# Optimization experiments

Hardware: AMD Instinct MI355X
Metric: run time of the kernel (lower is better)

The kernel has to match this reference:

```python
import jax, jax.numpy as jnp
import numpy as np

B, N, MODES, WIDTH = 4, 8192, 12, 32
TWO = 2 * MODES  # 24
M_TOT = TWO * (TWO - 1)  # 552


def setup_inputs() -> dict:
    key = jax.random.key(0)
    ks = jax.random.split(key, 12)
    scale = 1.0 / (WIDTH * WIDTH)
    x = jax.random.uniform(ks[0], (B, N, 2), jnp.float32)
    fc0_w = jax.random.normal(ks[1], (2, WIDTH), jnp.float32) * 0.1
    fc0_b = jax.random.normal(ks[2], (WIDTH,), jnp.float32) * 0.05
    # 4 layers x {weights1, weights2}, stored as real/imag pairs (torch.rand cfloat ~ U[0,1)+1j*U[0,1))
    spec_w = jax.random.uniform(ks[3], (4, 2, WIDTH, WIDTH, MODES, MODES, 2), jnp.float32) * scale
    conv_w = jax.random.normal(ks[4], (4, WIDTH, WIDTH), jnp.float32) * 0.1  # Conv1d k=1 -> [O,I]
    conv_b = jax.random.normal(ks[5], (4, WIDTH), jnp.float32) * 0.05
    fc1_w = jax.random.normal(ks[6], (WIDTH, 128), jnp.float32) * 0.1
    fc1_b = jax.random.normal(ks[7], (128,), jnp.float32) * 0.05
    fc2_w = jax.random.normal(ks[8], (128, 1), jnp.float32) * 0.1
    fc2_b = jax.random.normal(ks[9], (1,), jnp.float32) * 0.05
    return {"x": x, "fc0_w": fc0_w, "fc0_b": fc0_b, "spec_w": spec_w,
            "conv_w": conv_w, "conv_b": conv_b, "fc1_w": fc1_w, "fc1_b": fc1_b,
            "fc2_w": fc2_w, "fc2_b": fc2_b}


def _vft_matrices(xp, yp):
    # xp, yp: [B, N], already min-shifted and scaled to [0, 6.28]
    kx = jnp.concatenate([jnp.arange(MODES), jnp.arange(-MODES, 0)]).astype(jnp.float32)       # [24]
    ky = jnp.concatenate([jnp.arange(MODES), jnp.arange(-(MODES - 1), 0)]).astype(jnp.float32)  # [23]
    Xm = kx[None, :, None] * xp[:, None, :]  # [B,24,N]
    Ym = ky[None, :, None] * yp[:, None, :]  # [B,23,N]
    # torch: X repeat(1,23,1) tiles blocks; Y repeat(1,1,24).reshape interleaves -> row j*24+i = X[i]+Y[j]
    phase = jnp.tile(Xm, (1, TWO - 1, 1)) + jnp.repeat(Ym, TWO, axis=1)  # [B,552,N]
    V_fwd = jnp.exp(-1j * phase)                    # [B,552,N] complex64
    V_inv = jnp.conj(V_fwd).transpose(0, 2, 1)      # [B,N,552]
    return V_fwd, V_inv


def _spectral_conv(h, V_fwd, V_inv, w1, w2):
    # h: [B,C,N] real; w1,w2: [C,C,M,M] complex
    b, c, n = h.shape
    # forward Vandermonde transform: bmm(V_fwd, h^T) then permute -> [B,C,552]
    x_ft = jnp.einsum('bmn,bnc->bcm', V_fwd, h.astype(jnp.complex64).transpose(0, 2, 1))
    x_ft = x_ft.reshape(b, c, TWO, TWO - 1)
    top = jnp.einsum('bixy,ioxy->boxy', x_ft[:, :, :MODES, :MODES], w1)
    bot = jnp.einsum('bixy,ioxy->boxy', x_ft[:, :, -MODES:, :MODES], w2)
    out_ft = jnp.zeros((b, WIDTH, TWO, MODES), jnp.complex64)
    out_ft = out_ft.at[:, :, :MODES, :MODES].set(top)
    out_ft = out_ft.at[:, :, -MODES:, :MODES].set(bot)
    x_ft = out_ft.reshape(b, WIDTH, 2 * MODES * MODES)  # [B,C,288]
    # conjugate-symmetric completion (flip over last two dims, as in source)
    x_ft2 = jnp.conj(jnp.flip(x_ft[..., TWO:], axis=(-2, -1)))  # [B,C,264]
    x_ft = jnp.concatenate([x_ft, x_ft2], axis=-1)  # [B,C,552]
    out = jnp.einsum('bnm,bmc->bcn', V_inv, x_ft.transpose(0, 2, 1))  # [B,C,N]
    return (out / n * 2).real


def reference(x, fc0_w, fc0_b, spec_w, conv_w, conv_b, fc1_w, fc1_b, fc2_w, fc2_b):
    gelu = lambda t: jax.nn.gelu(t, approximate=False)
    # VFT mutates x in-place by subtracting global mins (view semantics in torch)
    xp = x[:, :, 0] - jnp.min(x[:, :, 0])
    yp = x[:, :, 1] - jnp.min(x[:, :, 1])
    x_in = jnp.stack([xp, yp], axis=-1)  # what fc0 actually sees
    V_fwd, V_inv = _vft_matrices(xp * 6.28 / jnp.max(xp), yp * 6.28 / jnp.max(yp))
    h = (x_in @ fc0_w + fc0_b).transpose(0, 2, 1)  # [B,C,N]
    for l in range(4):
        w1 = spec_w[l, 0, ..., 0] + 1j * spec_w[l, 0, ..., 1]
        w2 = spec_w[l, 1, ..., 0] + 1j * spec_w[l, 1, ..., 1]
        x1 = _spectral_conv(h, V_fwd, V_inv, w1, w2)
        x2 = jnp.einsum('bin,oi->bon', h, conv_w[l]) + conv_b[l][None, :, None]
        h = x1 + x2
        if l < 3:
            h = gelu(h)
    h = h.transpose(0, 2, 1)  # [B,N,C]
    h = gelu(h @ fc1_w + fc1_b)
    return h @ fc2_w + fc2_b  # [B,N,1]
```

## Files before the change

kernel.cpp:

```cpp
#include <hip/hip_runtime.h>
#include <cmath>

#define NB 4
#define NN 8192
#define CH 32

typedef short short8 __attribute__((ext_vector_type(8)));
typedef float floatx4 __attribute__((ext_vector_type(4)));
typedef unsigned short ushort_t;

__device__ __forceinline__ unsigned short f2b(float f){
  unsigned u = __float_as_uint(f);
  u = u + 0x7FFFu + ((u >> 16) & 1u);
  return (unsigned short)(u >> 16);
}
__device__ __forceinline__ float b2f(unsigned short h){
  return __uint_as_float(((unsigned)h) << 16);
}
__device__ __forceinline__ float gelu_f(float v){
  return 0.5f * v * (1.0f + erff(v * 0.70710678118654752440f));
}
__device__ __forceinline__ int repk(int t){
  int j = t / 24, i = t - j * 24;
  if(j == 0)  return (i <= 12) ? i : -1;
  if(j <= 11) return 13 + (j - 1) * 24 + i;
  return (i == 12) ? 277 + (j - 12) : -1;
}
__device__ __forceinline__ int partner(int t){
  int j = t / 24, i = t - j * 24;
  return ((23 - j) % 23) * 24 + ((24 - i) % 24);
}
__device__ __forceinline__ int repT(int k){
  if(k < 13) return k;
  if(k < 277){ int m = k - 13; return (m / 24 + 1) * 24 + (m % 24); }
  return (k - 277 + 12) * 24 + 12;
}

__global__ __launch_bounds__(256) void k_pre(const float* __restrict__ spec,
    float2* __restrict__ wt, const float* __restrict__ x, float4* __restrict__ pmm,
    const float* __restrict__ fc1w, ushort_t* __restrict__ WB,
    const float* __restrict__ convw, ushort_t* __restrict__ WA)
{
  const int tid = threadIdx.x;
  if(blockIdx.x < 128){
    int g = blockIdx.x * 256 + tid;
    float a = x[(size_t)g * 2], b = x[(size_t)g * 2 + 1];
    float mn0 = a, mx0 = a, mn1 = b, mx1 = b;
    for(int off = 32; off > 0; off >>= 1){
      mn0 = fminf(mn0, __shfl_down(mn0, off));
      mx0 = fmaxf(mx0, __shfl_down(mx0, off));
      mn1 = fminf(mn1, __shfl_down(mn1, off));
      mx1 = fmaxf(mx1, __shfl_down(mx1, off));
    }
    __shared__ float4 wp[4];
    if((tid & 63) == 0) wp[tid >> 6] = make_float4(mn0, mn1, mx0, mx1);
    __syncthreads();
    if(tid == 0){
      float4 r = wp[0];
      for(int i2 = 1; i2 < 4; ++i2){
        float4 v = wp[i2];
        r.x = fminf(r.x, v.x); r.y = fminf(r.y, v.y);
        r.z = fmaxf(r.z, v.z); r.w = fmaxf(r.w, v.w);
      }
      pmm[blockIdx.x] = r;
    }
  } else if(blockIdx.x < 4736){
    int g = (blockIdx.x - 128) * 256 + tid;
    int o  = g & 31;
    int i  = (g >> 5) & 31;
    int rest = g >> 10;
    int pq = rest % 144;
    int ls = rest / 144;
    wt[g] = ((const float2*)spec)[(((size_t)(ls * 32 + i) * 32 + o) * 144 + pq)];
  } else {
    for(int s = tid; s < 512; s += 256){
      int jt = s >> 6, l = s & 63;
      int c = l & 15, qq = l >> 4;
      #pragma unroll
      for(int e = 0; e < 8; ++e){
        float wv = fc1w[(qq * 8 + e) * 128 + jt * 16 + c];
        ushort_t hi = f2b(wv);
        WB[(jt * 64 + l) * 8 + e] = hi;
        WB[4096 + (jt * 64 + l) * 8 + e] = f2b(wv - b2f(hi));
      }
    }
    for(int s = tid; s < 8192; s += 256){
      int l2   = s >> 11;
      int rem  = s & 2047;
      int limb = rem >> 10;
      int rem2 = rem & 1023;
      int half = rem2 >> 9;
      int le   = rem2 & 511;
      int lane = le >> 3, e = le & 7;
      int c = half * 16 + (lane & 15);
      int i = (lane >> 4) * 8 + e;
      float wv = convw[((size_t)l2 * 32 + c) * 32 + i] * 4096.0f;
      ushort_t hi = f2b(wv);
      WA[s] = limb ? f2b(wv - b2f(hi)) : hi;
    }
  }
}

__global__ __launch_bounds__(256) void k_vbuild(const float* __restrict__ x,
    const float4* __restrict__ pmm, const float* __restrict__ fw,
    const float* __restrict__ fb, ushort_t* __restrict__ AF, ushort_t* __restrict__ VTF,
    ushort_t* __restrict__ hbB, ushort_t* __restrict__ hbChi, ushort_t* __restrict__ hbClo)
{
  __shared__ ushort_t lds1[32 * 584];
  __shared__ float4 mmv;
  const int tid = threadIdx.x;
  if(tid < 64){
    float4 a = pmm[tid], c = pmm[tid + 64];
    float mn0 = fminf(a.x, c.x), mn1 = fminf(a.y, c.y);
    float mx0 = fmaxf(a.z, c.z), mx1 = fmaxf(a.w, c.w);
    for(int off = 32; off > 0; off >>= 1){
      mn0 = fminf(mn0, __shfl_down(mn0, off));
      mn1 = fminf(mn1, __shfl_down(mn1, off));
      mx0 = fmaxf(mx0, __shfl_down(mx0, off));
      mx1 = fmaxf(mx1, __shfl_down(mx1, off));
    }
    if(tid == 0) mmv = make_float4(mn0, mn1, mx0, mx1);
  }
  __syncthreads();
  const int nl = tid & 31, part = tid >> 5;
  const int b = blockIdx.x >> 8;
  const int nblk = blockIdx.x & 255;
  const int n = nblk * 32 + nl;
  float mn0 = mmv.x, mn1 = mmv.y, mx0 = mmv.z, mx1 = mmv.w;
  float x0 = x[(size_t)(b * NN + n) * 2]     - mn0;
  float x1 = x[(size_t)(b * NN + n) * 2 + 1] - mn1;
  float sp = x0 * (6.28f / (mx0 - mn0));
  float sq = x1 * (6.28f / (mx1 - mn1));
  float cx, sx, cy, sy;
  sincosf(sp, &sx, &cx);
  sincosf(sq, &sy, &cy);
  int j0 = part * 3;
  int j1 = (j0 + 3 < 23) ? j0 + 3 : 23;
  float ky0 = (j0 < 12) ? (float)j0 : (float)(j0 - 23);
  float cb, sb;
  sincosf(ky0 * sq, &sb, &cb);
  for(int j = j0; j < j1; ++j){
    float ca = 1.0f, sa = 0.0f;
    #pragma unroll
    for(int i = 0; i < 24; ++i){
      float vr = ca * cb - sa * sb;
      float vi = -(sa * cb + ca * sb);
      int t = j * 24 + i;
      int k = repk(t);
      if(k >= 0){
        lds1[nl * 584 + k]       = f2b(vr);
        lds1[nl * 584 + 288 + k] = f2b(vi);
      }
      float cn = ca * cx - sa * sx;
      float sn = sa * cx + ca * sx;
      if(i == 11) sn = -sn;
      ca = cn; sa = sn;
    }
    float cbn = cb * cy - sb * sy;
    float sbn = sb * cy + cb * sy;
    cb = cbn; sb = sbn;
  }
  __syncthreads();
  #pragma unroll
  for(int r = 0; r < 9; ++r){
    int c = tid + 256 * r;
    int t16 = c / 1152;
    int c2 = c - t16 * 1152;
    int kk = c2 >> 6;
    int rem = c2 & 63;
    int q = rem >> 4, n15 = rem & 15;
    short8 v = *(const short8*)(lds1 + (t16 * 16 + n15) * 584 + kk * 32 + q * 8);
    *(short8*)(VTF + ((size_t)((b * 512 + nblk * 2 + t16) * 18 + kk)) * 512
               + (q * 16 + n15) * 8) = v;
  }
  #pragma unroll
  for(int r = 0; r < 9; ++r){
    int c = tid + 256 * r;
    int st = c >> 6;
    int rem = c & 63;
    int q = rem >> 4, srow = rem & 15;
    int sg = st * 16 + srow;
    int s = (sg < 288) ? sg : sg - 288;
    int sinh_ = (sg >= 288);
    int p2 = s / 12, qq = s - p2 * 12;
    int t = p2 * 23 + qq;
    int k = repk(t);
    unsigned short flip = 0;
    if(k < 0){ k = repk(partner(t)); if(sinh_) flip = 0x8000; }
    int col = sinh_ ? 288 + k : k;
    ushort_t tmp[8];
    #pragma unroll
    for(int e = 0; e < 8; ++e)
      tmp[e] = lds1[(q * 8 + e) * 584 + col] ^ flip;
    *(short8*)(AF + ((size_t)((b * 36 + st) * 256 + nblk)) * 512
               + (q * 16 + srow) * 8) = *(short8*)tmp;
  }
  #pragma unroll
  for(int rr = 0; rr < 4; ++rr){
    int c2 = part + rr * 8;
    float v = fb[c2] + x0 * fw[c2] + x1 * fw[32 + c2];
    ushort_t hi = f2b(v), lo = f2b(v - b2f(hi));
    int half = c2 >> 4, cl = c2 & 15;
    hbB[(((size_t)(b * 2 + half) * 256 + nblk) * 512) + ((nl >> 3) * 16 + cl) * 8 + (nl & 7)] = hi;
    size_t ca = ((size_t)(b * 512 + nblk * 2 + (nl >> 4))) * 512
              + ((c2 >> 3) * 16 + (nl & 15)) * 8 + (c2 & 7);
    hbChi[ca] = hi; hbClo[ca] = lo;
  }
}

__global__ __launch_bounds__(256) void k_fwd(const ushort_t* __restrict__ AF,
    const ushort_t* __restrict__ hbB, float* __restrict__ xp)
{
  const int stp = blockIdx.x;
  const int ks = blockIdx.y;
  const int b  = blockIdx.z;
  const int w = threadIdx.x >> 6;
  const int lane = threadIdx.x & 63;
  const int row = lane & 15;
  const int q = lane >> 4;
  const int st0 = stp * 2;
  const size_t abase0 = ((size_t)(b * 36 + st0) * 256) * 512 + (q * 16 + row) * 8;
  const size_t abase1 = abase0 + (size_t)256 * 512;
  const size_t hB0 = ((size_t)(b * 2 + 0) * 256) * 512 + (size_t)lane * 8;
  const size_t hB1 = ((size_t)(b * 2 + 1) * 256) * 512 + (size_t)lane * 8;
  floatx4 aA0 = {0.f,0.f,0.f,0.f}, aA1 = {0.f,0.f,0.f,0.f};
  floatx4 aB0 = {0.f,0.f,0.f,0.f}, aB1 = {0.f,0.f,0.f,0.f};
  #pragma unroll
  for(int kk = 0; kk < 4; ++kk){
    int g = ks * 16 + w * 4 + kk;
    short8 A0 = *(const short8*)(AF + abase0 + (size_t)g * 512);
    short8 A1 = *(const short8*)(AF + abase1 + (size_t)g * 512);
    short8 B0 = *(const short8*)(hbB + hB0 + (size_t)g * 512);
    short8 B1 = *(const short8*)(hbB + hB1 + (size_t)g * 512);
    aA0 = __builtin_amdgcn_mfma_f32_16x16x32_bf16(A0, B0, aA0, 0, 0, 0);
    aA1 = __builtin_amdgcn_mfma_f32_16x16x32_bf16(A0, B1, aA1, 0, 0, 0);
    aB0 = __builtin_amdgcn_mfma_f32_16x16x32_bf16(A1, B0, aB0, 0, 0, 0);
    aB1 = __builtin_amdgcn_mfma_f32_16x16x32_bf16(A1, B1, aB1, 0, 0, 0);
  }
  __shared__ float red[4 * 512];
  const int e = threadIdx.x;
  const int eo = e & 31;
  #pragma unroll
  for(int r = 0; r < 4; ++r){
    int rrow = q * 4 + r;
    red[w * 512 + rrow * 32 + row]      = aA0[r];
    red[w * 512 + rrow * 32 + 16 + row] = aA1[r];
  }
  __syncthreads();
  {
    float v0 = red[e] + red[512 + e] + red[1024 + e] + red[1536 + e];
    float v1 = red[e + 256] + red[512 + e + 256] + red[1024 + e + 256] + red[1536 + e + 256];
    size_t r0 = (size_t)(b * 576 + st0 * 16 + (e >> 5));
    xp[(r0 * 16 + ks) * 32 + eo]       = v0;
    xp[((r0 + 8) * 16 + ks) * 32 + eo] = v1;
  }
  __syncthreads();
  #pragma unroll
  for(int r = 0; r < 4; ++r){
    int rrow = q * 4 + r;
    red[w * 512 + rrow * 32 + row]      = aB0[r];
    red[w * 512 + rrow * 32 + 16 + row] = aB1[r];
  }
  __syncthreads();
  {
    float v0 = red[e] + red[512 + e] + red[1024 + e] + red[1536 + e];
    float v1 = red[e + 256] + red[512 + e + 256] + red[1024 + e + 256] + red[1536 + e + 256];
    size_t r0 = (size_t)(b * 576 + (st0 + 1) * 16 + (e >> 5));
    xp[(r0 * 16 + ks) * 32 + eo]       = v0;
    xp[((r0 + 8) * 16 + ks) * 32 + eo] = v1;
  }
}

__global__ __launch_bounds__(256) void k_mixg(const float* __restrict__ xp,
    const float2* __restrict__ wt, ushort_t* __restrict__ ghi, ushort_t* __restrict__ glof,
    int layer)
{
  const int w = threadIdx.x >> 6;
  const int lane = threadIdx.x & 63;
  const int k = blockIdx.x * 4 + w;
  const int b = blockIdx.y;
  const int t = repT(k);
  const int j = t / 24, i = t - j * 24;
  const int u = partner(t);
  const bool unpaired = (i == 12) || (u == t);
  const int idxT = (t < 288) ? t : 575 - t;  const bool cfT = (t >= 288);
  const int idxU = (u < 288) ? u : 575 - u;  const bool cfU = (u >= 288);
  __shared__ float Xs[4][2][64];
  #pragma unroll
  for(int m = 0; m < 2; ++m){
    int idx = m ? idxU : idxT;
    #pragma unroll
    for(int hf = 0; hf < 2; ++hf){
      int rrow = hf ? 288 + idx : idx;
      const float* sb = xp + (size_t)(b * 576 + rrow) * 512;
      float4 a = *(const float4*)(sb + lane * 4);
      float4 c = *(const float4*)(sb + 256 + lane * 4);
      a.x += c.x; a.y += c.y; a.z += c.z; a.w += c.w;
      #pragma unroll
      for(int mk = 8; mk <= 32; mk <<= 1){
        a.x += __shfl_xor(a.x, mk);
        a.y += __shfl_xor(a.y, mk);
        a.z += __shfl_xor(a.z, mk);
        a.w += __shfl_xor(a.w, mk);
      }
      if(lane < 8){
        int o0 = hf * 32 + lane * 4;
        Xs[w][m][o0 + 0] = a.x;
        Xs[w][m][o0 + 1] = a.y;
        Xs[w][m][o0 + 2] = a.z;
        Xs[w][m][o0 + 3] = a.w;
      }
    }
  }
  __syncthreads();
  const int o = lane & 31, half = lane >> 5;
  float Fr[2], Fi[2];
  #pragma unroll
  for(int m = 0; m < 2; ++m){
    int idx = m ? idxU : idxT;
    int p2 = idx / 12, qq = idx - p2 * 12;
    int sel = (p2 < 12) ? 0 : 1;
    int pq = (p2 % 12) * 12 + qq;
    const float2* wb = wt + ((size_t)((layer * 2 + sel) * 144 + pq)) * 1024;
    int i0 = half * 16;
    float fr = 0.f, fi = 0.f;
    #pragma unroll
    for(int ii = 0; ii < 16; ++ii){
      int i2 = i0 + ii;
      float xr = Xs[w][m][i2], xi = Xs[w][m][32 + i2];
      float2 wv = wb[i2 * 32 + o];
      fr += xr * wv.x - xi * wv.y;
      fi += xr * wv.y + xi * wv.x;
    }
    fr += __shfl_down(fr, 32);
    fi += __shfl_down(fi, 32);
    Fr[m] = fr; Fi[m] = fi;
  }
  const int c = lane & 31;
  const int srcT = cfT ? 31 - c : c;
  const int srcU = cfU ? 31 - c : c;
  float fax = __shfl(Fr[0], srcT);
  float fay = __shfl(Fi[0], srcT);
  float fbx = __shfl(Fr[1], srcU);
  float fby = __shfl(Fi[1], srcU);
  if(lane < 32){
    float gr = fax;
    float gi = cfT ? -fay : fay;
    if(!unpaired){
      gr += fbx;
      gi -= (cfU ? -fby : fby);
    }
    unsigned short hr = f2b(gr); float lr = gr - b2f(hr);
    unsigned short hi2 = f2b(gi); float li = gi - b2f(hi2);
    size_t base = (size_t)(b * CH + c) * 576;
    ghi[base + k] = hr;          ghi[base + 288 + k] = hi2;
    int hhc = c >> 4, cl = c & 15;
    int kk1 = k >> 5, q1 = (k >> 3) & 3, e1 = k & 7;
    size_t fb2 = (size_t)(b * 2 + hhc) * 18;
    glof[(fb2 + kk1) * 512 + (q1 * 16 + cl) * 8 + e1]     = f2b(lr);
    glof[(fb2 + 9 + kk1) * 512 + (q1 * 16 + cl) * 8 + e1] = f2b(li);
  }
}

template<int LAST>
__global__ __launch_bounds__(512, 6) void k_inv(const ushort_t* __restrict__ VTF,
    const ushort_t* __restrict__ ghi, const ushort_t* __restrict__ glof,
    const float* __restrict__ cbias, int layer,
    const ushort_t* __restrict__ hbCi_hi, const ushort_t* __restrict__ hbCi_lo,
    ushort_t* __restrict__ hbBo, ushort_t* __restrict__ hbCo_hi,
    ushort_t* __restrict__ hbCo_lo,
    const float* __restrict__ b1, const float* __restrict__ w2,
    const float* __restrict__ b2, float* __restrict__ out,
    const ushort_t* __restrict__ WBg, const ushort_t* __restrict__ WA)
{
  __shared__ ushort_t GH[32][584];
  const int tid = threadIdx.x;
  const int b = blockIdx.y;
  const int bx = blockIdx.x;
  for(int idx = tid; idx < 2304; idx += 512){
    int ch = idx / 72, g8 = (idx - ch * 72) * 8;
    if(g8 < 576)
      *(short8*)&GH[ch][g8] = *(const short8*)(ghi + (size_t)(b * CH + ch) * 576 + g8);
  }
  __syncthreads();
  const int lane = tid & 63;
  const int w = tid >> 6;
  const int tl = w >> 1;
  const int hh = w & 1;
  const int row = lane & 15, q = lane >> 4;
  const int t16 = bx * 4 + tl;
  const ushort_t* vb = VTF + ((size_t)(b * 512 + t16) * 18) * 512 + lane * 8;
  const ushort_t* gl = glof + ((size_t)(b * 2 + hh) * 18) * 512 + lane * 8;
  const int gr = hh * 16 + row, ko = q * 8;
  floatx4 ah = {0.f,0.f,0.f,0.f}, al = {0.f,0.f,0.f,0.f};
  #pragma unroll
  for(int kk = 0; kk < 18; ++kk){
    short8 Bv = *(const short8*)(vb + (size_t)kk * 512);
    short8 Ah = *(const short8*)&GH[gr][ko + kk * 32];
    short8 Al = *(const short8*)(gl + (size_t)kk * 512);
    ah = __builtin_amdgcn_mfma_f32_16x16x32_bf16(Ah, Bv, ah, 0, 0, 0);
    al = __builtin_amdgcn_mfma_f32_16x16x32_bf16(Al, Bv, al, 0, 0, 0);
  }
  {
    short8 Whi = *(const short8*)(WA + ((size_t)((layer * 2 + 0) * 2 + hh)) * 512 + lane * 8);
    short8 Wlo = *(const short8*)(WA + ((size_t)((layer * 2 + 1) * 2 + hh)) * 512 + lane * 8);
    short8 Bhi = *(const short8*)(hbCi_hi + ((size_t)(b * 512 + t16)) * 512 + lane * 8);
    short8 Blo = *(const short8*)(hbCi_lo + ((size_t)(b * 512 + t16)) * 512 + lane * 8);
    ah = __builtin_amdgcn_mfma_f32_16x16x32_bf16(Whi, Bhi, ah, 0, 0, 0);
    al = __builtin_amdgcn_mfma_f32_16x16x32_bf16(Wlo, Bhi, al, 0, 0, 0);
    ah = __builtin_amdgcn_mfma_f32_16x16x32_bf16(Whi, Blo, ah, 0, 0, 0);
  }
  floatx4 accF = ah + al;
  const float sc = 2.0f / 8192.0f;
  float cb[4];
  #pragma unroll
  for(int r = 0; r < 4; ++r) cb[r] = cbias[layer * 32 + hh * 16 + q * 4 + r];
  if constexpr(!LAST){
    const int n = bx * 64 + tl * 16 + row;
    const int g = n >> 5, qb = (n >> 3) & 3, e2 = n & 7;
    #pragma unroll
    for(int r = 0; r < 4; ++r){
      int c = hh * 16 + q * 4 + r;
      float v = gelu_f(accF[r] * sc + cb[r]);
      ushort_t hi = f2b(v), lo = f2b(v - b2f(hi));
      hbBo[(((size_t)(b * 2 + hh) * 256 + g) * 512) + (qb * 16 + (q * 4 + r)) * 8 + e2] = hi;
      size_t ca = ((size_t)(b * 512 + t16)) * 512 + ((c >> 3) * 16 + row) * 8 + (c & 7);
      hbCo_hi[ca] = hi; hbCo_lo[ca] = lo;
    }
  } else {
    __shared__ ushort_t hHi[64][36];
    __shared__ ushort_t hLo[64][36];
    __shared__ float part[2][64];
    {
      ushort_t H[4], L[4];
      #pragma unroll
      for(int r = 0; r < 4; ++r){
        float v = accF[r] * sc + cb[r];
        H[r] = f2b(v); L[r] = f2b(v - b2f(H[r]));
      }
      uint2 uu;
      uu.x = (unsigned)H[0] | ((unsigned)H[1] << 16);
      uu.y = (unsigned)H[2] | ((unsigned)H[3] << 16);
      *(uint2*)&hHi[tl * 16 + row][hh * 16 + q * 4] = uu;
      uu.x = (unsigned)L[0] | ((unsigned)L[1] << 16);
      uu.y = (unsigned)L[2] | ((unsigned)L[3] << 16);
      *(uint2*)&hLo[tl * 16 + row][hh * 16 + q * 4] = uu;
    }
    __syncthreads();
    const int cl = row;
    short8 Ahi = *(const short8*)&hHi[tl * 16 + cl][q * 8];
    short8 Alo = *(const short8*)&hLo[tl * 16 + cl][q * 8];
    float S0 = 0.f, S1 = 0.f, S2 = 0.f, S3 = 0.f;
    #pragma unroll
    for(int jt2 = 0; jt2 < 4; ++jt2){
      int jt = hh * 4 + jt2;
      short8 Bhi = *(const short8*)(WBg + (jt * 64 + lane) * 8);
      short8 Blo = *(const short8*)(WBg + 4096 + (jt * 64 + lane) * 8);
      floatx4 acc = {0.f, 0.f, 0.f, 0.f};
      acc = __builtin_amdgcn_mfma_f32_16x16x32_bf16(Ahi, Bhi, acc, 0, 0, 0);
      acc = __builtin_amdgcn_mfma_f32_16x16x32_bf16(Alo, Bhi, acc, 0, 0, 0);
      acc = __builtin_amdgcn_mfma_f32_16x16x32_bf16(Ahi, Blo, acc, 0, 0, 0);
      float bv = b1[jt * 16 + cl], wv = w2[jt * 16 + cl];
      S0 = fmaf(gelu_f(acc[0] + bv), wv, S0);
      S1 = fmaf(gelu_f(acc[1] + bv), wv, S1);
      S2 = fmaf(gelu_f(acc[2] + bv), wv, S2);
      S3 = fmaf(gelu_f(acc[3] + bv), wv, S3);
    }
    #pragma unroll
    for(int off = 8; off; off >>= 1){
      S0 += __shfl_xor(S0, off, 16);
      S1 += __shfl_xor(S1, off, 16);
      S2 += __shfl_xor(S2, off, 16);
      S3 += __shfl_xor(S3, off, 16);
    }
    if(cl == 0){
      int pb = tl * 16 + q * 4;
      part[hh][pb + 0] = S0;
      part[hh][pb + 1] = S1;
      part[hh][pb + 2] = S2;
      part[hh][pb + 3] = S3;
    }
    __syncthreads();
    if(tid < 64)
      out[(size_t)b * NN + bx * 64 + tid] = part[0][tid] + part[1][tid] + b2[0];
  }
}

extern "C" void kernel_launch(void* const* d_in, const int* in_sizes, int n_in,
                              void* d_out, int out_size, void* d_ws, size_t ws_size,
                              hipStream_t stream)
{
  const float* x      = (const float*)d_in[0];
  const float* fc0_w  = (const float*)d_in[1];
  const float* fc0_b  = (const float*)d_in[2];
  const float* spec_w = (const float*)d_in[3];
  const float* conv_w = (const float*)d_in[4];
  const float* conv_b = (const float*)d_in[5];
  const float* fc1_w  = (const float*)d_in[6];
  const float* fc1_b  = (const float*)d_in[7];
  const float* fc2_w  = (const float*)d_in[8];
  const float* fc2_b  = (const float*)d_in[9];
  float* out = (float*)d_out;

  char* w = (char*)d_ws;
  const size_t OFF_PMM  = 0;
  const size_t OFF_WT   = 4096;
  const size_t OFF_AF   = OFF_WT  + 9437184;
  const size_t OFF_VTF  = OFF_AF  + 37748736;
  const size_t OFF_HB0  = OFF_VTF + 37748736;
  const size_t OFF_HB1  = OFF_HB0 + 2097152;
  const size_t OFF_HC0  = OFF_HB1 + 2097152;
  const size_t OFF_HC1  = OFF_HC0 + 2097152;
  const size_t OFF_HL0  = OFF_HC1 + 2097152;
  const size_t OFF_HL1  = OFF_HL0 + 2097152;
  const size_t OFF_XP   = OFF_HL1 + 2097152;
  const size_t OFF_GHI  = OFF_XP  + 4718592;
  const size_t OFF_GLO  = OFF_GHI + 147456;
  const size_t OFF_WB   = OFF_GLO + 147456;
  const size_t OFF_WA   = OFF_WB  + 16384;

  float4* pmm    = (float4*)(w + OFF_PMM);
  float2* wt     = (float2*)(w + OFF_WT);
  ushort_t* AF   = (ushort_t*)(w + OFF_AF);
  ushort_t* VTF  = (ushort_t*)(w + OFF_VTF);
  ushort_t* hbB[2]  = { (ushort_t*)(w + OFF_HB0), (ushort_t*)(w + OFF_HB1) };
  ushort_t* hbChi[2] = { (ushort_t*)(w + OFF_HC0), (ushort_t*)(w + OFF_HC1) };
  ushort_t* hbClo[2] = { (ushort_t*)(w + OFF_HL0), (ushort_t*)(w + OFF_HL1) };
  float* xp      = (float*)(w + OFF_XP);
  ushort_t* ghi  = (ushort_t*)(w + OFF_GHI);
  ushort_t* glof = (ushort_t*)(w + OFF_GLO);
  ushort_t* WB   = (ushort_t*)(w + OFF_WB);
  ushort_t* WA   = (ushort_t*)(w + OFF_WA);

  hipLaunchKernelGGL(k_pre, dim3(4737), dim3(256), 0, stream, spec_w, wt, x, pmm,
                     fc1_w, WB, conv_w, WA);
  hipLaunchKernelGGL(k_vbuild, dim3(1024), dim3(256), 0, stream, x, pmm,
                     fc0_w, fc0_b, AF, VTF, hbB[0], hbChi[0], hbClo[0]);

  for(int l = 0; l < 4; ++l){
    int in = l & 1, outb = 1 - in;
    hipLaunchKernelGGL(k_fwd, dim3(18, 16, NB), dim3(256), 0, stream, AF, hbB[in], xp);
    hipLaunchKernelGGL(k_mixg, dim3(72, NB), dim3(256), 0, stream, xp, wt, ghi, glof, l);
    if(l < 3)
      hipLaunchKernelGGL(k_inv<0>, dim3(128, NB), dim3(512), 0, stream, VTF, ghi, glof,
                         conv_b, l, hbChi[in], hbClo[in],
                         hbB[outb], hbChi[outb], hbClo[outb],
                         fc1_b, fc2_w, fc2_b, out, WB, WA);
    else
      hipLaunchKernelGGL(k_inv<1>, dim3(128, NB), dim3(512), 0, stream, VTF, ghi, glof,
                         conv_b, l, hbChi[in], hbClo[in],
                         hbB[outb], hbChi[outb], hbClo[outb],
                         fc1_b, fc2_w, fc2_b, out, WB, WA);
  }
  (void)in_sizes; (void)n_in; (void)out_size; (void)ws_size;
}
```

Baseline: 226.5 us.

## Split k_mixg mode work across four waves per block to raise parallelism

```diff
diff --git a/kernel.cpp b/kernel.cpp
--- a/kernel.cpp
+++ b/kernel.cpp
@@ -275,9 +275,9 @@
     const float2* __restrict__ wt, ushort_t* __restrict__ ghi, ushort_t* __restrict__ glof,
     int layer)
 {
-  const int w = threadIdx.x >> 6;
+  const int wv = threadIdx.x >> 6;
   const int lane = threadIdx.x & 63;
-  const int k = blockIdx.x * 4 + w;
+  const int k = blockIdx.x;
   const int b = blockIdx.y;
   const int t = repT(k);
   const int j = t / 24, i = t - j * 24;
@@ -285,65 +285,62 @@
   const bool unpaired = (i == 12) || (u == t);
   const int idxT = (t < 288) ? t : 575 - t;  const bool cfT = (t >= 288);
   const int idxU = (u < 288) ? u : 575 - u;  const bool cfU = (u >= 288);
-  __shared__ float Xs[4][2][64];
-  #pragma unroll
-  for(int m = 0; m < 2; ++m){
+  __shared__ float Xs[2][64];
+  __shared__ float FrP[2][2][32], FiP[2][2][32];
+  {
+    const int m = wv & 1, hf = wv >> 1;
     int idx = m ? idxU : idxT;
+    int rrow = hf ? 288 + idx : idx;
+    const float* sb = xp + (size_t)(b * 576 + rrow) * 512;
+    float4 a = *(const float4*)(sb + lane * 4);
+    float4 c = *(const float4*)(sb + 256 + lane * 4);
+    a.x += c.x; a.y += c.y; a.z += c.z; a.w += c.w;
     #pragma unroll
-    for(int hf = 0; hf < 2; ++hf){
-      int rrow = hf ? 288 + idx : idx;
-      const float* sb = xp + (size_t)(b * 576 + rrow) * 512;
-      float4 a = *(const float4*)(sb + lane * 4);
-      float4 c = *(const float4*)(sb + 256 + lane * 4);
-      a.x += c.x; a.y += c.y; a.z += c.z; a.w += c.w;
-      #pragma unroll
-      for(int mk = 8; mk <= 32; mk <<= 1){
-        a.x += __shfl_xor(a.x, mk);
-        a.y += __shfl_xor(a.y, mk);
-        a.z += __shfl_xor(a.z, mk);
-        a.w += __shfl_xor(a.w, mk);
-      }
-      if(lane < 8){
-        int o0 = hf * 32 + lane * 4;
-        Xs[w][m][o0 + 0] = a.x;
-        Xs[w][m][o0 + 1] = a.y;
-        Xs[w][m][o0 + 2] = a.z;
-        Xs[w][m][o0 + 3] = a.w;
-      }
-    }
-  }
-  __syncthreads();
-  const int o = lane & 31, half = lane >> 5;
-  float Fr[2], Fi[2];
-  #pragma unroll
-  for(int m = 0; m < 2; ++m){
+    for(int mk = 8; mk <= 32; mk <<= 1){
+      a.x += __shfl_xor(a.x, mk);
+      a.y += __shfl_xor(a.y, mk);
+      a.z += __shfl_xor(a.z, mk);
+      a.w += __shfl_xor(a.w, mk);
+    }
+    if(lane < 8){
+      int o0 = hf * 32 + lane * 4;
+      Xs[m][o0 + 0] = a.x;
+      Xs[m][o0 + 1] = a.y;
+      Xs[m][o0 + 2] = a.z;
+      Xs[m][o0 + 3] = a.w;
+    }
+  }
+  __syncthreads();
+  {
+    const int m = wv & 1, ih = wv >> 1;
     int idx = m ? idxU : idxT;
     int p2 = idx / 12, qq = idx - p2 * 12;
     int sel = (p2 < 12) ? 0 : 1;
     int pq = (p2 % 12) * 12 + qq;
     const float2* wb = wt + ((size_t)((layer * 2 + sel) * 144 + pq)) * 1024;
-    int i0 = half * 16;
-    float fr = 0.f, fi = 0.f;
-    #pragma unroll
-    for(int ii = 0; ii < 16; ++ii){
-      int i2 = i0 + ii;
-      float xr = Xs[w][m][i2], xi = Xs[w][m][32 + i2];
-      float2 wv = wb[i2 * 32 + o];
-      fr += xr * wv.x - xi * wv.y;
-      fi += xr * wv.y + xi * wv.x;
-    }
-    fr += __shfl_down(fr, 32);
-    fi += __shfl_down(fi, 32);
-    Fr[m] = fr; Fi[m] = fi;
-  }
-  const int c = lane & 31;
-  const int srcT = cfT ? 31 - c : c;
-  const int srcU = cfU ? 31 - c : c;
-  float fax = __shfl(Fr[0], srcT);
-  float fay = __shfl(Fi[0], srcT);
-  float fbx = __shfl(Fr[1], srcU);
-  float fby = __shfl(Fi[1], srcU);
-  if(lane < 32){
+    if(lane < 32){
+      const int o = lane;
+      float fr = 0.f, fi = 0.f;
+      #pragma unroll
+      for(int ii = 0; ii < 16; ++ii){
+        int i2 = ih * 16 + ii;
+        float xr = Xs[m][i2], xi = Xs[m][32 + i2];
+        float2 wvv = wb[i2 * 32 + o];
+        fr += xr * wvv.x - xi * wvv.y;
+        fi += xr * wvv.y + xi * wvv.x;
+      }
+      FrP[m][ih][o] = fr; FiP[m][ih][o] = fi;
+    }
+  }
+  __syncthreads();
+  if(wv == 0 && lane < 32){
+    const int c = lane;
+    const int srcT = cfT ? 31 - c : c;
+    const int srcU = cfU ? 31 - c : c;
+    float fax = FrP[0][0][srcT] + FrP[0][1][srcT];
+    float fay = FiP[0][0][srcT] + FiP[0][1][srcT];
+    float fbx = FrP[1][0][srcU] + FrP[1][1][srcU];
+    float fby = FiP[1][0][srcU] + FiP[1][1][srcU];
     float gr = fax;
     float gi = cfT ? -fay : fay;
     if(!unpaired){
@@ -540,7 +537,7 @@
   for(int l = 0; l < 4; ++l){
     int in = l & 1, outb = 1 - in;
     hipLaunchKernelGGL(k_fwd, dim3(18, 16, NB), dim3(256), 0, stream, AF, hbB[in], xp);
-    hipLaunchKernelGGL(k_mixg, dim3(72, NB), dim3(256), 0, stream, xp, wt, ghi, glof, l);
+    hipLaunchKernelGGL(k_mixg, dim3(288, NB), dim3(256), 0, stream, xp, wt, ghi, glof, l);
     if(l < 3)
       hipLaunchKernelGGL(k_inv<0>, dim3(128, NB), dim3(512), 0, stream, VTF, ghi, glof,
                          conv_b, l, hbChi[in], hbClo[in],
```

After: 224.2 us. Within noise of the previous version (-1.0%).
